# Kernel tuning notes

Measured on AMD Instinct MI355X. Metric: run time of the kernel, lower is better.

The kernel has to match this reference:

```python
import jax, jax.numpy as jnp
import numpy as np

NUM_HEADS = 8
HEAD_DIM = 64
FEATURES = 512
LN_EPS = 1e-5


def setup_inputs() -> dict:
    key = jax.random.key(0)
    ks = jax.random.split(key, 8)
    b, n = 4, 2048
    mid = NUM_HEADS * HEAD_DIM
    q = jax.random.normal(ks[0], (b, n, mid), dtype=jnp.float32)
    k = jax.random.normal(ks[1], (b, n, mid), dtype=jnp.float32)
    v = jax.random.normal(ks[2], (b, n, mid), dtype=jnp.float32)
    mask = jax.random.randint(ks[3], (b, n), 0, 2) > 0
    attention_bias = jax.random.normal(ks[4], (b, NUM_HEADS, n, n + 1), dtype=jnp.float32)
    tokens = jax.random.normal(ks[5], (2, HEAD_DIM), dtype=jnp.float32)  # null k/v tokens
    w_out = jax.random.normal(ks[6], (FEATURES, mid), dtype=jnp.float32) / np.sqrt(mid)
    gamma = jnp.ones((FEATURES,), dtype=jnp.float32)
    return {"q": q, "k": k, "v": v, "mask": mask, "attention_bias": attention_bias,
            "tokens": tokens, "w_out": w_out, "gamma": gamma}


def _attention(q, k, v, mask, attention_bias, tokens, w_out, gamma):
    b, n, _ = q.shape
    h, d = NUM_HEADS, HEAD_DIM
    # b n (h d) -> b h n d
    qh = q.reshape(b, n, h, d).transpose(0, 2, 1, 3) * (d ** -0.5)
    kh = k.reshape(b, n, h, d).transpose(0, 2, 1, 3)
    vh = v.reshape(b, n, h, d).transpose(0, 2, 1, 3)
    # insert null tokens at position 0 of key/value sequence
    nk = jnp.broadcast_to(tokens[0], (b, h, 1, d))
    nv = jnp.broadcast_to(tokens[1], (b, h, 1, d))
    kh = jnp.concatenate([nk, kh], axis=2)  # b h (n+1) d
    vh = jnp.concatenate([nv, vh], axis=2)
    sim = jnp.einsum('bhid,bhjd->bhij', qh, kh) + attention_bias
    # pad mask with True for the null token, broadcast b 1 1 j
    m = jnp.pad(mask, ((0, 0), (1, 0)), constant_values=True)[:, None, None, :]
    max_neg = -jnp.finfo(sim.dtype).max
    sim = jnp.where(m, sim, max_neg)
    attn = jax.nn.softmax(sim.astype(jnp.float32), axis=-1).astype(vh.dtype)
    out = jnp.einsum('bhij,bhjd->bhid', attn, vh)
    out = out.transpose(0, 2, 1, 3).reshape(b, n, h * d)  # b n (h d)
    out = out @ w_out.T  # Linear, no bias
    # CenteredLayerNorm: learned gamma, zero beta
    mu = jnp.mean(out, axis=-1, keepdims=True)
    var = jnp.mean(jnp.square(out - mu), axis=-1, keepdims=True)
    return (out - mu) * jax.lax.rsqrt(var + LN_EPS) * gamma


def reference(q, k, v, mask, attention_bias, tokens, w_out, gamma):
    return _attention(q, k, v, mask, attention_bias, tokens, w_out, gamma)
```

## Files before the change

kernel.cpp:

```cpp
#include <hip/hip_runtime.h>

typedef __bf16 bf16_t;
typedef __bf16 bf16x8 __attribute__((ext_vector_type(8)));
typedef float f32x4 __attribute__((ext_vector_type(4)));

#define MFMA(a, b, c) __builtin_amdgcn_mfma_f32_16x16x32_bf16(a, b, c, 0, 0, 0)

constexpr int NH  = 8;
constexpr int HD  = 64;
constexpr int SEQ = 2048;
constexpr int MID = 512;

__device__ __forceinline__ bf16x8 ld8(const void* base, long e, bool isb) {
    if (isb) return *(const bf16x8*)((const bf16_t*)base + e);
    const float* f = (const float*)base + e;
    bf16x8 r;
#pragma unroll
    for (int j = 0; j < 8; ++j) r[j] = (bf16_t)f[j];
    return r;
}
__device__ __forceinline__ float ld1(const void* base, long e, bool isb) {
    return isb ? (float)((const bf16_t*)base)[e] : ((const float*)base)[e];
}
__device__ __forceinline__ void st1(void* base, long e, float v, bool isb) {
    if (isb) ((bf16_t*)base)[e] = (bf16_t)v;
    else     ((float*)base)[e]  = v;
}
__device__ __forceinline__ bool detect_bf16(const void* gamma) {
    return *(const unsigned*)gamma == 0x3F803F80u;
}

__global__ __launch_bounds__(256) void attn_kernel(
    const void* __restrict__ q, const void* __restrict__ k,
    const void* __restrict__ v, const int* __restrict__ mask,
    const void* __restrict__ bias, const void* __restrict__ tokens,
    const void* __restrict__ gamma, void* __restrict__ d_out,
    void* __restrict__ d_ws)
{
    const bool isb = detect_bf16(gamma);
    bf16_t* attn_out = isb ? (bf16_t*)d_out : (bf16_t*)d_ws;

    __shared__ __align__(16) bf16_t Ks[64][72];
    __shared__ __align__(16) bf16_t Vt[64][72];
    __shared__ __align__(16) bf16_t Pl[4][16][72];
    __shared__ int Ml[64];

    const int tid  = threadIdx.x;
    const int lane = tid & 63;
    const int wave = tid >> 6;
    const int c    = lane & 15;
    const int quad = lane >> 4;

    const int qt = blockIdx.x & 31;
    const int bh = blockIdx.x >> 5;
    const int h  = bh & 7;
    const int b  = bh >> 3;

    const int qbase = qt * 64 + wave * 16;

    const long qoff = (long)(b * SEQ + qbase + c) * MID + h * HD;
    bf16x8 qa0 = ld8(q, qoff + quad * 8, isb);
    bf16x8 qa1 = ld8(q, qoff + quad * 8 + 32, isb);
#pragma unroll
    for (int j = 0; j < 8; ++j) {
        qa0[j] = (bf16_t)((float)qa0[j] * 0.125f);
        qa1[j] = (bf16_t)((float)qa1[j] * 0.125f);
    }

    const long boff = (long)bh * SEQ * (SEQ + 1);
    const long brow0 = boff + (long)(qbase + quad * 4) * (SEQ + 1);

    bf16x8 nb0 = {}; bf16x8 nb1 = {};
    if (c == 0) {
#pragma unroll
        for (int j = 0; j < 8; ++j) {
            nb0[j] = (bf16_t)ld1(tokens, quad * 8 + j, isb);
            nb1[j] = (bf16_t)ld1(tokens, 32 + quad * 8 + j, isb);
        }
    }
    f32x4 z = {0.f, 0.f, 0.f, 0.f};
    f32x4 s0 = MFMA(qa0, nb0, z);
    s0 = MFMA(qa1, nb1, s0);

    float m_i[4], l_i[4];
    f32x4 O[4];
#pragma unroll
    for (int r = 0; r < 4; ++r) {
        float sn = __shfl(s0[r], 0, 16) + ld1(bias, brow0 + (long)r * (SEQ + 1), isb);
        m_i[r] = sn;
        l_i[r] = 1.0f;
    }
#pragma unroll
    for (int d = 0; d < 4; ++d) {
        float vn = ld1(tokens, 64 + d * 16 + c, isb);
        O[d] = {vn, vn, vn, vn};
    }

    for (int kb = 0; kb < SEQ / 64; ++kb) {
#pragma unroll
        for (int it = 0; it < 2; ++it) {
            int idx = tid + it * 256;
            int key = idx >> 3;
            int dof = (idx & 7) * 8;
            long g = (long)(b * SEQ + kb * 64 + key) * MID + h * HD + dof;
            *(bf16x8*)&Ks[key][dof] = ld8(k, g, isb);
            bf16x8 vv = ld8(v, g, isb);
#pragma unroll
            for (int j = 0; j < 8; ++j) Vt[dof + j][key] = vv[j];
        }
        if (tid < 64) Ml[tid] = mask[b * SEQ + kb * 64 + tid];
        __syncthreads();

        float sv[4][4];
#pragma unroll
        for (int t = 0; t < 4; ++t) {
            int col = t * 16 + c;
            long bcol = 1 + (long)kb * 64 + col;
            f32x4 acc;
#pragma unroll
            for (int r = 0; r < 4; ++r)
                acc[r] = ld1(bias, brow0 + (long)r * (SEQ + 1) + bcol, isb);
            bf16x8 kf0 = *(const bf16x8*)&Ks[col][quad * 8];
            bf16x8 kf1 = *(const bf16x8*)&Ks[col][quad * 8 + 32];
            acc = MFMA(qa0, kf0, acc);
            acc = MFMA(qa1, kf1, acc);
            bool ok = Ml[col] != 0;
#pragma unroll
            for (int r = 0; r < 4; ++r) sv[t][r] = ok ? acc[r] : -1e30f;
        }

        float alpha[4];
#pragma unroll
        for (int r = 0; r < 4; ++r) {
            float mx = fmaxf(fmaxf(sv[0][r], sv[1][r]), fmaxf(sv[2][r], sv[3][r]));
#pragma unroll
            for (int off = 1; off < 16; off <<= 1) mx = fmaxf(mx, __shfl_xor(mx, off));
            float mnew = fmaxf(m_i[r], mx);
            alpha[r] = __expf(m_i[r] - mnew);
            float ps = 0.f;
#pragma unroll
            for (int t = 0; t < 4; ++t) {
                float p = __expf(sv[t][r] - mnew);
                sv[t][r] = p;
                ps += p;
            }
#pragma unroll
            for (int off = 1; off < 16; off <<= 1) ps += __shfl_xor(ps, off);
            l_i[r] = l_i[r] * alpha[r] + ps;
            m_i[r] = mnew;
        }

#pragma unroll
        for (int t = 0; t < 4; ++t)
#pragma unroll
            for (int r = 0; r < 4; ++r)
                Pl[wave][quad * 4 + r][t * 16 + c] = (bf16_t)sv[t][r];
        __syncthreads();

        bf16x8 pa0 = *(const bf16x8*)&Pl[wave][c][quad * 8];
        bf16x8 pa1 = *(const bf16x8*)&Pl[wave][c][quad * 8 + 32];
#pragma unroll
        for (int d = 0; d < 4; ++d) {
            bf16x8 vf0 = *(const bf16x8*)&Vt[d * 16 + c][quad * 8];
            bf16x8 vf1 = *(const bf16x8*)&Vt[d * 16 + c][quad * 8 + 32];
            f32x4 o = O[d];
#pragma unroll
            for (int r = 0; r < 4; ++r) o[r] *= alpha[r];
            o = MFMA(pa0, vf0, o);
            o = MFMA(pa1, vf1, o);
            O[d] = o;
        }
        __syncthreads();
    }

#pragma unroll
    for (int r = 0; r < 4; ++r) {
        float rl = 1.0f / l_i[r];
        long orow = (long)(b * SEQ + qbase + quad * 4 + r) * MID + h * HD;
#pragma unroll
        for (int d = 0; d < 4; ++d)
            attn_out[orow + d * 16 + c] = (bf16_t)(O[d][r] * rl);
    }
}

__global__ __launch_bounds__(256) void proj_ln_kernel(
    const void* __restrict__ w, const void* __restrict__ gamma,
    void* __restrict__ d_out, void* __restrict__ d_ws)
{
    const bool isb = detect_bf16(gamma);
    const bf16_t* x = isb ? (const bf16_t*)d_out : (const bf16_t*)d_ws;

    __shared__ float red[2][4][16];
    const int tid  = threadIdx.x;
    const int lane = tid & 63;
    const int wave = tid >> 6;
    const int c    = lane & 15;
    const int quad = lane >> 4;
    const int rb   = blockIdx.x * 16;
    const int cbase = wave * 128;

    f32x4 acc[8];
#pragma unroll
    for (int t = 0; t < 8; ++t) acc[t] = {0.f, 0.f, 0.f, 0.f};

    const bf16_t* xrow = x + (long)(rb + c) * MID;

    for (int kc = 0; kc < 16; ++kc) {
        bf16x8 a = *(const bf16x8*)(xrow + kc * 32 + quad * 8);
#pragma unroll
        for (int t = 0; t < 8; ++t) {
            long we = (long)(cbase + t * 16 + c) * MID + kc * 32 + quad * 8;
            bf16x8 bf = ld8(w, we, isb);
            acc[t] = MFMA(a, bf, acc[t]);
        }
    }

    float ls[4], lq[4];
#pragma unroll
    for (int r = 0; r < 4; ++r) {
        float s = 0.f, ss = 0.f;
#pragma unroll
        for (int t = 0; t < 8; ++t) { float vv = acc[t][r]; s += vv; ss += vv * vv; }
#pragma unroll
        for (int off = 1; off < 16; off <<= 1) { s += __shfl_xor(s, off); ss += __shfl_xor(ss, off); }
        ls[r] = s; lq[r] = ss;
    }
    if (c == 0) {
#pragma unroll
        for (int r = 0; r < 4; ++r) {
            red[0][wave][quad * 4 + r] = ls[r];
            red[1][wave][quad * 4 + r] = lq[r];
        }
    }
    __syncthreads();

#pragma unroll
    for (int r = 0; r < 4; ++r) {
        int row = quad * 4 + r;
        float S  = red[0][0][row] + red[0][1][row] + red[0][2][row] + red[0][3][row];
        float Q2 = red[1][0][row] + red[1][1][row] + red[1][2][row] + red[1][3][row];
        float mu  = S * (1.0f / 512.0f);
        float var = Q2 * (1.0f / 512.0f) - mu * mu;
        float rstd = rsqrtf(var + 1e-5f);
        long orow = (long)(rb + row) * MID;
#pragma unroll
        for (int t = 0; t < 8; ++t) {
            int col = cbase + t * 16 + c;
            float g = ld1(gamma, col, isb);
            st1(d_out, orow + col, (acc[t][r] - mu) * rstd * g, isb);
        }
    }
}

extern "C" void kernel_launch(void* const* d_in, const int* in_sizes, int n_in,
                              void* d_out, int out_size, void* d_ws, size_t ws_size,
                              hipStream_t stream)
{
    const void* q      = d_in[0];
    const void* k      = d_in[1];
    const void* v      = d_in[2];
    const int*  mask   = (const int*)d_in[3];
    const void* bias   = d_in[4];
    const void* tokens = d_in[5];
    const void* w_out  = d_in[6];
    const void* gamma  = d_in[7];

    attn_kernel<<<dim3(4 * NH * (SEQ / 64)), dim3(256), 0, stream>>>(
        q, k, v, mask, bias, tokens, gamma, d_out, d_ws);
    proj_ln_kernel<<<dim3((4 * SEQ) / 16), dim3(256), 0, stream>>>(
        w_out, gamma, d_out, d_ws);
}
```

Baseline: 950.2 us.

## Vectorize loads, prefetch bias, swizzle V tile, pre-convert weights, drop sync

Float-to-bf16 conversion loads now use 16-byte vector reads. The attention bias for each key block is prefetched into registers before the K/V tile is staged. The transposed V tile in shared memory gets an XOR swizzle to cut bank conflicts, and the intra-iteration __syncthreads is replaced by a scheduling barrier, since each wave only reads its own P rows. A new small kernel converts w_out to bf16 once into workspace so the projection GEMM reads bf16 directly, and gamma loads are hoisted. Dropping the barrier relies on per-wave LDS ordering within the wave.

```diff
diff --git a/kernel.cpp b/kernel.cpp
--- a/kernel.cpp
+++ b/kernel.cpp
@@ -10,24 +10,33 @@
 constexpr int HD  = 64;
 constexpr int SEQ = 2048;
 constexpr int MID = 512;
-
-__device__ __forceinline__ bf16x8 ld8(const void* base, long e, bool isb) {
+constexpr size_t WB_OFF = (size_t)4 * SEQ * MID * sizeof(bf16_t);
+
+__device__ __forceinline__ bool detect_bf16(const void* gamma) {
+    return *(const unsigned*)gamma == 0x3F803F80u;
+}
+__device__ __forceinline__ bf16x8 ld8v(const void* base, long e, bool isb) {
     if (isb) return *(const bf16x8*)((const bf16_t*)base + e);
     const float* f = (const float*)base + e;
+    f32x4 a = *(const f32x4*)f;
+    f32x4 b = *(const f32x4*)(f + 4);
     bf16x8 r;
 #pragma unroll
-    for (int j = 0; j < 8; ++j) r[j] = (bf16_t)f[j];
+    for (int j = 0; j < 4; ++j) { r[j] = (bf16_t)a[j]; r[4 + j] = (bf16_t)b[j]; }
     return r;
 }
 __device__ __forceinline__ float ld1(const void* base, long e, bool isb) {
     return isb ? (float)((const bf16_t*)base)[e] : ((const float*)base)[e];
 }
-__device__ __forceinline__ void st1(void* base, long e, float v, bool isb) {
-    if (isb) ((bf16_t*)base)[e] = (bf16_t)v;
-    else     ((float*)base)[e]  = v;
-}
-__device__ __forceinline__ bool detect_bf16(const void* gamma) {
-    return *(const unsigned*)gamma == 0x3F803F80u;
+
+__global__ __launch_bounds__(256) void wconv_kernel(
+    const void* __restrict__ w, const void* __restrict__ gamma,
+    void* __restrict__ d_ws)
+{
+    const bool isb = detect_bf16(gamma);
+    bf16_t* wb = (bf16_t*)((char*)d_ws + WB_OFF);
+    const int i = (blockIdx.x * 256 + threadIdx.x) * 8;
+    *(bf16x8*)(wb + i) = ld8v(w, i, isb);
 }
 
 __global__ __launch_bounds__(256) void attn_kernel(
@@ -59,8 +68,8 @@
     const int qbase = qt * 64 + wave * 16;
 
     const long qoff = (long)(b * SEQ + qbase + c) * MID + h * HD;
-    bf16x8 qa0 = ld8(q, qoff + quad * 8, isb);
-    bf16x8 qa1 = ld8(q, qoff + quad * 8 + 32, isb);
+    bf16x8 qa0 = ld8v(q, qoff + quad * 8, isb);
+    bf16x8 qa1 = ld8v(q, qoff + quad * 8 + 32, isb);
 #pragma unroll
     for (int j = 0; j < 8; ++j) {
         qa0[j] = (bf16_t)((float)qa0[j] * 0.125f);
@@ -72,11 +81,8 @@
 
     bf16x8 nb0 = {}; bf16x8 nb1 = {};
     if (c == 0) {
-#pragma unroll
-        for (int j = 0; j < 8; ++j) {
-            nb0[j] = (bf16_t)ld1(tokens, quad * 8 + j, isb);
-            nb1[j] = (bf16_t)ld1(tokens, 32 + quad * 8 + j, isb);
-        }
+        nb0 = ld8v(tokens, quad * 8, isb);
+        nb1 = ld8v(tokens, 32 + quad * 8, isb);
     }
     f32x4 z = {0.f, 0.f, 0.f, 0.f};
     f32x4 s0 = MFMA(qa0, nb0, z);
@@ -97,16 +103,38 @@
     }
 
     for (int kb = 0; kb < SEQ / 64; ++kb) {
+        float bw[4][4];
+        {
+            const long b0 = brow0 + 1 + (long)kb * 64 + c;
+            if (isb) {
+                const bf16_t* bp = (const bf16_t*)bias;
+#pragma unroll
+                for (int t = 0; t < 4; ++t)
+#pragma unroll
+                    for (int r = 0; r < 4; ++r)
+                        bw[t][r] = (float)bp[b0 + (long)r * (SEQ + 1) + t * 16];
+            } else {
+                const float* bp = (const float*)bias;
+#pragma unroll
+                for (int t = 0; t < 4; ++t)
+#pragma unroll
+                    for (int r = 0; r < 4; ++r)
+                        bw[t][r] = bp[b0 + (long)r * (SEQ + 1) + t * 16];
+            }
+        }
+
 #pragma unroll
         for (int it = 0; it < 2; ++it) {
             int idx = tid + it * 256;
             int key = idx >> 3;
-            int dof = (idx & 7) * 8;
+            int m   = idx & 7;
+            int dof = m * 8;
             long g = (long)(b * SEQ + kb * 64 + key) * MID + h * HD + dof;
-            *(bf16x8*)&Ks[key][dof] = ld8(k, g, isb);
-            bf16x8 vv = ld8(v, g, isb);
-#pragma unroll
-            for (int j = 0; j < 8; ++j) Vt[dof + j][key] = vv[j];
+            *(bf16x8*)&Ks[key][dof] = ld8v(k, g, isb);
+            bf16x8 vv = ld8v(v, g, isb);
+            int kcol = key ^ (m << 3);
+#pragma unroll
+            for (int j = 0; j < 8; ++j) Vt[dof + j][kcol] = vv[j];
         }
         if (tid < 64) Ml[tid] = mask[b * SEQ + kb * 64 + tid];
         __syncthreads();
@@ -115,11 +143,9 @@
 #pragma unroll
         for (int t = 0; t < 4; ++t) {
             int col = t * 16 + c;
-            long bcol = 1 + (long)kb * 64 + col;
             f32x4 acc;
 #pragma unroll
-            for (int r = 0; r < 4; ++r)
-                acc[r] = ld1(bias, brow0 + (long)r * (SEQ + 1) + bcol, isb);
+            for (int r = 0; r < 4; ++r) acc[r] = bw[t][r];
             bf16x8 kf0 = *(const bf16x8*)&Ks[col][quad * 8];
             bf16x8 kf1 = *(const bf16x8*)&Ks[col][quad * 8 + 32];
             acc = MFMA(qa0, kf0, acc);
@@ -155,14 +181,16 @@
 #pragma unroll
             for (int r = 0; r < 4; ++r)
                 Pl[wave][quad * 4 + r][t * 16 + c] = (bf16_t)sv[t][r];
-        __syncthreads();
+        __builtin_amdgcn_sched_barrier(0);
 
         bf16x8 pa0 = *(const bf16x8*)&Pl[wave][c][quad * 8];
         bf16x8 pa1 = *(const bf16x8*)&Pl[wave][c][quad * 8 + 32];
 #pragma unroll
         for (int d = 0; d < 4; ++d) {
-            bf16x8 vf0 = *(const bf16x8*)&Vt[d * 16 + c][quad * 8];
-            bf16x8 vf1 = *(const bf16x8*)&Vt[d * 16 + c][quad * 8 + 32];
+            int vr = d * 16 + c;
+            int sw = ((vr >> 3) & 7) << 3;
+            bf16x8 vf0 = *(const bf16x8*)&Vt[vr][(quad * 8) ^ sw];
+            bf16x8 vf1 = *(const bf16x8*)&Vt[vr][(32 + quad * 8) ^ sw];
             f32x4 o = O[d];
 #pragma unroll
             for (int r = 0; r < 4; ++r) o[r] *= alpha[r];
@@ -184,11 +212,12 @@
 }
 
 __global__ __launch_bounds__(256) void proj_ln_kernel(
-    const void* __restrict__ w, const void* __restrict__ gamma,
-    void* __restrict__ d_out, void* __restrict__ d_ws)
+    const void* __restrict__ gamma, void* __restrict__ d_out,
+    void* __restrict__ d_ws)
 {
     const bool isb = detect_bf16(gamma);
-    const bf16_t* x = isb ? (const bf16_t*)d_out : (const bf16_t*)d_ws;
+    const bf16_t* x  = isb ? (const bf16_t*)d_out : (const bf16_t*)d_ws;
+    const bf16_t* wb = (const bf16_t*)((const char*)d_ws + WB_OFF);
 
     __shared__ float red[2][4][16];
     const int tid  = threadIdx.x;
@@ -209,9 +238,8 @@
         bf16x8 a = *(const bf16x8*)(xrow + kc * 32 + quad * 8);
 #pragma unroll
         for (int t = 0; t < 8; ++t) {
-            long we = (long)(cbase + t * 16 + c) * MID + kc * 32 + quad * 8;
-            bf16x8 bf = ld8(w, we, isb);
-            acc[t] = MFMA(a, bf, acc[t]);
+            const bf16_t* wp = wb + (long)(cbase + t * 16 + c) * MID + kc * 32 + quad * 8;
+            acc[t] = MFMA(a, *(const bf16x8*)wp, acc[t]);
         }
     }
 
@@ -231,6 +259,17 @@
             red[0][wave][quad * 4 + r] = ls[r];
             red[1][wave][quad * 4 + r] = lq[r];
         }
+    }
+
+    float gv[8];
+    if (isb) {
+        const bf16_t* gp = (const bf16_t*)gamma;
+#pragma unroll
+        for (int t = 0; t < 8; ++t) gv[t] = (float)gp[cbase + t * 16 + c];
+    } else {
+        const float* gp = (const float*)gamma;
+#pragma unroll
+        for (int t = 0; t < 8; ++t) gv[t] = gp[cbase + t * 16 + c];
     }
     __syncthreads();
 
@@ -243,11 +282,18 @@
         float var = Q2 * (1.0f / 512.0f) - mu * mu;
         float rstd = rsqrtf(var + 1e-5f);
         long orow = (long)(rb + row) * MID;
-#pragma unroll
-        for (int t = 0; t < 8; ++t) {
-            int col = cbase + t * 16 + c;
-            float g = ld1(gamma, col, isb);
-            st1(d_out, orow + col, (acc[t][r] - mu) * rstd * g, isb);
+        if (isb) {
+#pragma unroll
+            for (int t = 0; t < 8; ++t) {
+                int col = cbase + t * 16 + c;
+                ((bf16_t*)d_out)[orow + col] = (bf16_t)((acc[t][r] - mu) * rstd * gv[t]);
+            }
+        } else {
+#pragma unroll
+            for (int t = 0; t < 8; ++t) {
+                int col = cbase + t * 16 + c;
+                ((float*)d_out)[orow + col] = (acc[t][r] - mu) * rstd * gv[t];
+            }
         }
     }
 }
@@ -265,8 +311,9 @@
     const void* w_out  = d_in[6];
     const void* gamma  = d_in[7];
 
+    wconv_kernel<<<dim3(128), dim3(256), 0, stream>>>(w_out, gamma, d_ws);
     attn_kernel<<<dim3(4 * NH * (SEQ / 64)), dim3(256), 0, stream>>>(
         q, k, v, mask, bias, tokens, gamma, d_out, d_ws);
     proj_ln_kernel<<<dim3((4 * SEQ) / 16), dim3(256), 0, stream>>>(
-        w_out, gamma, d_out, d_ws);
-}
+        gamma, d_out, d_ws);
+}
```

After: 866.0 us. -8.9%, faster.
